# Optimization experiments

Measured on AMD Instinct MI355X. Metric: run time of the kernel, lower is better.

## Reference

```python
import jax, jax.numpy as jnp
import numpy as np

MAXDISP = 192  # must match init_kwargs max_disp


def _interp_axis(x, axis, out_size):
    """1-D linear interpolation along `axis` with align_corners=True."""
    in_size = x.shape[axis]
    src = jnp.arange(out_size, dtype=jnp.float32) * ((in_size - 1) / (out_size - 1))
    i0 = jnp.clip(jnp.floor(src).astype(jnp.int32), 0, in_size - 1)
    i1 = jnp.clip(i0 + 1, 0, in_size - 1)
    w = (src - i0.astype(jnp.float32)).astype(x.dtype)
    shape = [1] * x.ndim
    shape[axis] = out_size
    w = w.reshape(shape)
    return jnp.take(x, i0, axis=axis) * (1 - w) + jnp.take(x, i1, axis=axis) * w


def create_cost_volume(left, right, maxdisp):
    """Vectorized version of the original per-disparity slice-copy loop.
    cost[:, :C, d, :, w] = left[:, :, :, w]        if w >= d else 0
    cost[:, C:, d, :, w] = right[:, :, :, w - d]   if w >= d else 0
    Returns [B, 2C, D, H, W] with D = maxdisp // 4.
    """
    B, C, H, W = left.shape
    D = maxdisp // 4
    d = jnp.arange(D)[:, None]          # [D,1]
    w = jnp.arange(W)[None, :]          # [1,W]
    mask = (w >= d).astype(left.dtype)  # [D,W]
    idx = jnp.clip(w - d, 0, W - 1)     # [D,W] shifted gather indices
    mask_b = mask[None, None, :, None, :]                       # [1,1,D,1,W]
    cost_left = left[:, :, None, :, :] * mask_b                 # [B,C,D,H,W]
    cost_right = jnp.take(right, idx.reshape(-1), axis=3)       # [B,C,H,D*W]
    cost_right = cost_right.reshape(B, C, H, D, W)
    cost_right = jnp.transpose(cost_right, (0, 1, 3, 2, 4)) * mask_b
    return jnp.concatenate([cost_left, cost_right], axis=1)     # [B,2C,D,H,W]


def upsample_regression(vol, maxdisp):
    """Trilinear x4 upsample (align_corners=True) + softmax over disparity +
    soft-argmin expectation. vol: [B, D/4, H/4, W/4] -> [B, H, W]."""
    x = vol
    for axis in (1, 2, 3):
        x = _interp_axis(x, axis, x.shape[axis] * 4)
    p = jax.nn.softmax(x, axis=1)                       # [B, maxdisp, H, W]
    disps = jnp.arange(maxdisp, dtype=x.dtype)
    return jnp.einsum('bdhw,d->bhw', p, disps)


def setup_inputs() -> dict:
    key = jax.random.key(0)
    k1, k2 = jax.random.split(key)
    left = jax.random.normal(k1, (2, 32, 64, 128), dtype=jnp.float32)
    right = jax.random.normal(k2, (2, 32, 64, 128), dtype=jnp.float32)
    return {"left": left, "right": right}


def reference(left, right):
    cost = create_cost_volume(left, right, MAXDISP)  # [B,2C,D,H,W]
    # Stand-in for the (unavailable) stacked hourglass 3D-CNN: channel mean
    # reduces the cost volume to a single-channel disparity volume [B,D,H,W].
    vol = cost.mean(axis=1)
    return upsample_regression(vol, MAXDISP)  # [B, 4H, 4W]
```

## Files before the change

### kernel.cpp

```cpp
#include <hip/hip_runtime.h>

#define BB 2
#define CC 32
#define HC 64
#define WC 128
#define HO 256
#define WO 512
#define MAXD 192
#define NBLK (BB * HO)
#define RPAD 47
#define RSZ  176

#define QUARTER(K, MASKED)                                                     \
  {                                                                            \
    constexpr int DDLO = 48 * (K);                                             \
    constexpr int DDHI = DDLO + 47;                                            \
    constexpr int DLO  = (DDLO * 47) / 191;                                    \
    constexpr int DHI  = (DDHI * 47) / 191;                                    \
    constexpr int NV   = DHI - DLO + 2;                                        \
    float vv[NV];                                                              \
    _Pragma("unroll")                                                          \
    for (int j = 0; j < NV; ++j) {                                             \
      int d = DLO + j;                                                         \
      if (d > 47) {                                                            \
        vv[j] = vv[j - 1];                    \
      } else {                                                                 \
        float t0 = Rhp[RPAD + w0 - d];               \
        float t1 = Rhp[RPAD + w0 - d + 1];           \
        float bn;                                                              \
        if (MASKED) {                                                          \
          float df = (float)d;                                                 \
          bn = fmaf(cB0, __saturatef(w0f - df + 1.f),                          \
                    cB1 * __saturatef(w0f - df + 2.f));                        \
        } else {                                                               \
          bn = cA;                                                             \
        }                                                                      \
        vv[j] = fmaf(c0, t0, fmaf(c1, t1, bn));                                \
      }                                                                        \
    }                                                                          \
    _Pragma("unroll")                                                          \
    for (int j = DLO; j <= DHI; ++j) {                                         \
      int dd0 = (191 * j + 46) / 47;  if (dd0 < DDLO) dd0 = DDLO;              \
      int dd1 = (191 * j + 190) / 47; if (dd1 > DDHI) dd1 = DDHI;              \
      float s   = vv[j - DLO + 1] - vv[j - DLO];                               \
      float wd0 = (float)dd0 * (47.0f / 191.0f) - (float)j;                    \
      float e   = __builtin_amdgcn_exp2f(fmaf(wd0, s, vv[j - DLO]));           \
      float rr  = 1.f;                                                         \
      if (dd1 > dd0) rr = __builtin_amdgcn_exp2f(s * (47.0f / 191.0f));        \
      _Pragma("unroll")                                                        \
      for (int dd = dd0; dd <= dd1; ++dd) {                                    \
        if (dd & 1) { ls1 += e; ss1 = fmaf(e, (float)dd, ss1); }               \
        else        { ls0 += e; ss0 = fmaf(e, (float)dd, ss0); }               \
        if (dd < dd1) e *= rr;                                                 \
      }                                                                        \
    }                                                                          \
  }

__global__ __launch_bounds__(512)
__attribute__((amdgpu_waves_per_eu(4, 4)))
void fused_disp_kernel(const float* __restrict__ left,
                       const float* __restrict__ right,
                       float* __restrict__ out) {
    __shared__ float4 red[2][8][32];
    __shared__ float  Lh[WC];
    __shared__ float  Rhp[RSZ];

    int blk = blockIdx.x;
    int r   = (blk & 7) * (NBLK / 8) + (blk >> 3);
    int b   = r >> 8;
    int hh  = r & (HO - 1);

    float src_h = (float)hh * (63.0f / 255.0f);
    int h0 = (int)src_h; if (h0 > HC - 1) h0 = HC - 1;
    int h1 = h0 + 1;     if (h1 > HC - 1) h1 = HC - 1;
    float fh = src_h - (float)h0;

    int t = threadIdx.x;

    {
        int mat = t >> 8;
        int u   = t & 255;
        int cg  = u >> 5;
        int wq  = u & 31;
        const float* srcp = (mat ? right : left) + (size_t)b * (CC * HC * WC);
        float ax = 0.f, ay = 0.f, az = 0.f, aw = 0.f;
        float bx = 0.f, by = 0.f, bz = 0.f, bw = 0.f;
#pragma unroll
        for (int i = 0; i < 4; ++i) {
            int c = cg * 4 + i;
            float4 v0 = *(const float4*)(srcp + ((c * HC + h0) * WC + wq * 4));
            float4 v1 = *(const float4*)(srcp + ((c * HC + h1) * WC + wq * 4));
            ax += v0.x; ay += v0.y; az += v0.z; aw += v0.w;
            bx += v1.x; by += v1.y; bz += v1.z; bw += v1.w;
        }
        float gh = 1.f - fh;
        red[mat][cg][wq] = make_float4(fmaf(gh, ax, fh * bx), fmaf(gh, ay, fh * by),
                                       fmaf(gh, az, fh * bz), fmaf(gh, aw, fh * bw));
    }
    __syncthreads();
    if (t < 256) {
        int mat = t >> 7;
        int w   = t & 127;
        const float* redf = (const float*)red;
        float s = 0.f;
#pragma unroll
        for (int cgi = 0; cgi < 8; ++cgi) s += redf[(mat * 8 + cgi) * 128 + w];
        if (mat == 0) Lh[w] = s;
        else          Rhp[RPAD + w] = s;
    } else {
        int z = t - 256;
        if (z < RPAD)       Rhp[z] = 0.f;
        else if (z == RPAD) Rhp[RSZ - 1] = 0.f;
    }
    __syncthreads();

    int ww = t;
    float src_w = (float)ww * (127.0f / 511.0f);
    int w0 = (int)src_w; if (w0 > WC - 1) w0 = WC - 1;
    int w1 = w0 + 1;     if (w1 > WC - 1) w1 = WC - 1;
    float fw = src_w - (float)w0;

    const float L2E_SC = 1.4426950408889634f / 64.0f;
    float c0  = (1.f - fw) * L2E_SC;
    float c1  = fw * L2E_SC;
    float lw0 = Lh[w0], lw1 = Lh[w1];
    float cB0 = c0 * lw0, cB1 = c1 * lw1;
    float cA  = cB0 + cB1;
    float w0f = (float)w0;

    float ls0 = 0.f, ls1 = 0.f, ss0 = 0.f, ss1 = 0.f;
    if (t < 192) {
        QUARTER(0, true)
        QUARTER(1, true)
        QUARTER(2, true)
        QUARTER(3, true)
    } else {
        QUARTER(0, false)
        QUARTER(1, false)
        QUARTER(2, false)
        QUARTER(3, false)
    }

    out[(size_t)r * WO + ww] = (ss0 + ss1) / (ls0 + ls1);
}

extern "C" void kernel_launch(void* const* d_in, const int* in_sizes, int n_in,
                              void* d_out, int out_size, void* d_ws, size_t ws_size,
                              hipStream_t stream) {
    const float* left  = (const float*)d_in[0];
    const float* right = (const float*)d_in[1];
    fused_disp_kernel<<<NBLK, 512, 0, stream>>>(left, right, (float*)d_out);
}
```

Before: 63.89 us.

## Split each output row across two blocks and disparity halves across threads

Each block now handles half an output row (256 columns), and the two 256-thread halves of the block split the disparity range, each taking two of the four quarters. Partial softmax sums are combined through shared memory before the division and store. Occupancy hint raised to 8 waves per EU. This doubles the grid and shortens the serial per-thread exp loop, at the cost of recomputing the channel/height reduction twice per row, plus an extra barrier and extra shared memory.

```diff
diff --git a/kernel.cpp b/kernel.cpp
--- a/kernel.cpp
+++ b/kernel.cpp
@@ -7,7 +7,7 @@
 #define HO 256
 #define WO 512
 #define MAXD 192
-#define NBLK (BB * HO)
+#define NBLK2 1024
 #define RPAD 47
 #define RSZ  176
 
@@ -57,16 +57,20 @@
   }
 
 __global__ __launch_bounds__(512)
-__attribute__((amdgpu_waves_per_eu(4, 4)))
+__attribute__((amdgpu_waves_per_eu(8, 8)))
 void fused_disp_kernel(const float* __restrict__ left,
                        const float* __restrict__ right,
                        float* __restrict__ out) {
     __shared__ float4 red[2][8][32];
     __shared__ float  Lh[WC];
     __shared__ float  Rhp[RSZ];
+    __shared__ float  redL[2][256];
+    __shared__ float  redS[2][256];
 
     int blk = blockIdx.x;
-    int r   = (blk & 7) * (NBLK / 8) + (blk >> 3);
+    int u   = (blk & 7) * (NBLK2 / 8) + (blk >> 3);
+    int r   = u >> 1;
+    int g   = u & 1;
     int b   = r >> 8;
     int hh  = r & (HO - 1);
 
@@ -79,9 +83,9 @@
 
     {
         int mat = t >> 8;
-        int u   = t & 255;
-        int cg  = u >> 5;
-        int wq  = u & 31;
+        int uu  = t & 255;
+        int cg  = uu >> 5;
+        int wq  = uu & 31;
         const float* srcp = (mat ? right : left) + (size_t)b * (CC * HC * WC);
         float ax = 0.f, ay = 0.f, az = 0.f, aw = 0.f;
         float bx = 0.f, by = 0.f, bz = 0.f, bw = 0.f;
@@ -114,7 +118,10 @@
     }
     __syncthreads();
 
-    int ww = t;
+    int p  = t & 255;
+    int k  = t >> 8;
+    int ww = g * 256 + p;
+
     float src_w = (float)ww * (127.0f / 511.0f);
     int w0 = (int)src_w; if (w0 > WC - 1) w0 = WC - 1;
     int w1 = w0 + 1;     if (w1 > WC - 1) w1 = WC - 1;
@@ -129,19 +136,22 @@
     float w0f = (float)w0;
 
     float ls0 = 0.f, ls1 = 0.f, ss0 = 0.f, ss1 = 0.f;
-    if (t < 192) {
-        QUARTER(0, true)
-        QUARTER(1, true)
-        QUARTER(2, true)
-        QUARTER(3, true)
+    if (k == 0) {
+        if (g == 0 && p < 192) { QUARTER(0, true)  QUARTER(1, true)  }
+        else                   { QUARTER(0, false) QUARTER(1, false) }
     } else {
-        QUARTER(0, false)
-        QUARTER(1, false)
-        QUARTER(2, false)
-        QUARTER(3, false)
+        if (g == 0 && p < 192) { QUARTER(2, true)  QUARTER(3, true)  }
+        else                   { QUARTER(2, false) QUARTER(3, false) }
     }
+    redL[k][p] = ls0 + ls1;
+    redS[k][p] = ss0 + ss1;
+    __syncthreads();
 
-    out[(size_t)r * WO + ww] = (ss0 + ss1) / (ls0 + ls1);
+    if (t < 256) {
+        float ls = redL[0][t] + redL[1][t];
+        float ss = redS[0][t] + redS[1][t];
+        out[(size_t)r * WO + g * 256 + t] = ss / ls;
+    }
 }
 
 extern "C" void kernel_launch(void* const* d_in, const int* in_sizes, int n_in,
@@ -149,5 +159,5 @@
                               hipStream_t stream) {
     const float* left  = (const float*)d_in[0];
     const float* right = (const float*)d_in[1];
-    fused_disp_kernel<<<NBLK, 512, 0, stream>>>(left, right, (float*)d_out);
+    fused_disp_kernel<<<NBLK2, 512, 0, stream>>>(left, right, (float*)d_out);
 }
```

After: 66.00 us. +3.3%, slower.
